# Optimization experiments

Measured on AMD Instinct MI355X. Metric: run time of the kernel, lower is better.

## Reference

```python
import jax, jax.numpy as jnp
import numpy as np

# ---- constants mirroring the torch module ----
OSAMP = 8            # temporal oversampling factor
MAX_ITER = 10        # forward solver iterations (LBFGS replaced by fixed GD)
NEG_SHIFT = 2 * OSAMP
OTP = 5              # baseline frames subtracted from ctc/aif
C_SHARP = 500.0      # sharpness constant C=500 in fermi_ir_func
LR = 0.1             # fixed step size for the deterministic forward solve


def interp_linear_1d(x, size):
    # interp_linear_1D: linear upsampling along last (time) axis
    return jax.image.resize(x, x.shape[:-1] + (size,), method='linear')


def fermi_ir(eta, t_os):
    # eta: [B,3,H,W] = (amplitude A, decay rate k, delay t0); t_os: [Tos]
    tsh = t_os - t_os[NEG_SHIFT]                    # negative time shift
    A = eta[:, 0][..., None]                        # [B,H,W,1]
    k = eta[:, 1][..., None]
    t0 = eta[:, 2][..., None]
    step = jax.nn.sigmoid(C_SHARP * tsh)            # sharp causal onset (C=500)
    return A * jax.nn.sigmoid(k * (t0 - tsh)) * step  # [B,H,W,Tos]


def convolve(aif, ir):
    # linear convolution along time via FFT; output aligned with neg_shift offset
    Tos = ir.shape[-1]
    n = 2 * Tos
    Fa = jnp.fft.rfft(aif, n=n, axis=-1)            # [B,1,1,n/2+1]
    Fi = jnp.fft.rfft(ir, n=n, axis=-1)             # [B,H,W,n/2+1]
    full = jnp.fft.irfft(Fa * Fi, n=n, axis=-1)
    return jax.lax.dynamic_slice_in_dim(full, NEG_SHIFT, Tos, axis=-1)


def make_objective(ctc, aif, time, eta_prior, lambda_reg):
    # preprocessing from FermiDataConsLBFGS.forward
    aif = aif - aif[..., :OTP].mean(-1, keepdims=True)
    ctc = ctc - ctc[..., :OTP].mean(-1, keepdims=True)
    Tos = OSAMP * ctc.shape[-1]
    aif_os = interp_linear_1d(aif, Tos)
    ctc_os = interp_linear_1d(ctc, Tos)
    t_os = interp_linear_1d(time, Tos)
    ctc_dc = ctc_os[..., ::OSAMP]                   # [B,H,W,T]
    C_nn = (eta_prior ** 2).sum(axis=(0, 2, 3), keepdims=True)  # [1,3,1,1]
    C_dc = (ctc_dc ** 2).sum()
    sp_lam = jax.nn.softplus(lambda_reg).squeeze()

    def F_obj(eta):  # FermiDConsObj.__call__ (OD disabled: indx_dc = all frames)
        ir = fermi_ir(eta, t_os)
        ctc_est = convolve(aif_os, ir)[..., ::OSAMP] / OSAMP
        dc = ((ctc_dc - ctc_est) ** 2 / C_dc).sum()
        reg = sp_lam * (((eta - eta_prior) ** 2) / C_nn).sum()
        pos = (jax.nn.relu(-eta) ** 2).sum()
        return dc + reg + pos
    return F_obj


def setup_inputs():
    key = jax.random.key(0)
    k1, k2, k3, k4 = jax.random.split(key, 4)
    B, H, W, T = 1, 128, 128, 64
    ctc = jax.random.normal(k1, (B, H, W, T), jnp.float32) * 0.1
    aif = jax.random.uniform(k2, (B, 1, 1, T), jnp.float32)
    time = jnp.arange(T, dtype=jnp.float32)
    seg = jnp.ones((B, H, W), jnp.int32)
    eta_nn = jax.random.uniform(k3, (B, 3, H, W), jnp.float32)
    lambda_reg = jax.random.normal(k4, (1,), jnp.float32)
    return {"ctc": ctc, "aif": aif, "time": time, "seg": seg,
            "eta_nn": eta_nn, "lambda_reg": lambda_reg}


def reference(ctc, aif, time, seg, eta_nn, lambda_reg):
    # seg only affects the (disabled) outlier-detection path
    F_obj = make_objective(ctc, aif, time, eta_nn, lambda_reg)
    gradF = jax.grad(F_obj)

    def step(eta, _):
        return eta - LR * gradF(eta), None

    eta_pi, _ = jax.lax.scan(step, eta_nn, None, length=MAX_ITER)
    return eta_pi
```

## Files before the change

### kernel.cpp

```cpp
#include <hip/hip_runtime.h>
#include <math.h>

#define T_IN 64
#define NPIX 16384
#define MAX_ITER 10
#define NSLOT 43

typedef _Float16 half8_t __attribute__((ext_vector_type(8)));
typedef __fp16   fp16x2  __attribute__((ext_vector_type(2)));
typedef float    f32x4   __attribute__((ext_vector_type(4)));
typedef int      i32x4   __attribute__((ext_vector_type(4)));

union H8 { half8_t v; fp16x2 h2[4]; i32x4 i4; };

__device__ __forceinline__ float rcp_fast(float x) { return __builtin_amdgcn_rcpf(x); }

__constant__ constexpr int NTMIN[16] = {0,0,0,0,0,1,1,1,1,2,2,2,2,3,3,3};
__constant__ constexpr int TOFS[16]  = {0,4,8,12,16,20,23,26,29,32,34,36,38,40,41,42};

template<int KT>
__device__ __forceinline__ void buildTile(float T0, float nK, float r, int q,
        const float (&d10b)[16], const float (&tse0)[8], const float (&tse15)[8],
        H8& F0h, H8& F1h, H8& F2h) {
    float  x[8];
    fp16x2 d1h[4];
    float  d10 = T0 - d10b[KT];
    const fp16x2 c1 = {(__fp16)0.25f, (__fp16)0.25f};
    const fp16x2 c2 = {(__fp16)0.50f, (__fp16)0.50f};
    const fp16x2 c3 = {(__fp16)0.75f, (__fp16)0.75f};
    bool arith = true;
    if constexpr (KT == 0 || KT == 15) {
        bool flat = (KT == 0) ? (q == 0) : (q == 3);
        if (flat) {
            arith = false;
            const float* te;
            if constexpr (KT == 0) te = tse0; else te = tse15;
            #pragma unroll
            for (int j = 0; j < 8; ++j) x[j] = __expf(nK * (T0 - te[j]));
            #pragma unroll
            for (int jj = 0; jj < 4; ++jj)
                d1h[jj] = __builtin_amdgcn_cvt_pkrtz(T0 - te[2*jj],
                                                     T0 - te[2*jj+1]);
        }
    }
    if (arith) {
        x[0] = __expf(nK * d10);
        x[4] = __expf(nK * (d10 - 0.5f));
        x[1] = x[0]*r; x[2] = x[1]*r; x[3] = x[2]*r;
        x[5] = x[4]*r; x[6] = x[5]*r; x[7] = x[6]*r;
        fp16x2 D0 = __builtin_amdgcn_cvt_pkrtz(d10, d10 - 0.125f);
        d1h[0] = D0;
        d1h[1] = D0 - c1;
        d1h[2] = D0 - c2;
        d1h[3] = D0 - c3;
    }
    #pragma unroll
    for (int jj = 0; jj < 4; ++jj) {
        float s1a = rcp_fast(1.0f + x[2*jj]);
        float s1b = rcp_fast(1.0f + x[2*jj+1]);
        fp16x2 sh = __builtin_amdgcn_cvt_pkrtz(s1a, s1b);
        fp16x2 eh = sh - sh*sh;
        F0h.h2[jj] = sh;
        F1h.h2[jj] = eh * d1h[jj];
        F2h.h2[jj] = eh;
    }
}

template<int KT>
struct Pipe2 {
    static __device__ __forceinline__ void run(float T0, float nK, float r, int q, int lane,
            const float (&d10b)[16], const float (&tse0)[8], const float (&tse15)[8],
            const i32x4* __restrict__ Bs,
            H8 (&F0p)[2], H8 (&F1p)[2], H8 (&F2p)[2],
            f32x4 (&acc)[3][4]) {
        constexpr int PB = (KT >> 1) & 1;
        if constexpr (KT + 2 < 16)
            buildTile<KT+2>(T0, nK, r, q, d10b, tse0, tse15,
                            F0p[PB^1], F1p[PB^1], F2p[PB^1]);
        const f32x4 Z = (f32x4){0.f, 0.f, 0.f, 0.f};
        #pragma unroll
        for (int nt = NTMIN[KT]; nt < 4; ++nt) {
            int slot = TOFS[KT] + nt - NTMIN[KT];
            H8 bh; bh.i4 = Bs[slot*64 + lane];
            if constexpr (KT < 2) {
                acc[0][nt] = __builtin_amdgcn_mfma_f32_16x16x32_f16(F0p[PB].v, bh.v, Z, 0, 0, 0);
                acc[1][nt] = __builtin_amdgcn_mfma_f32_16x16x32_f16(F1p[PB].v, bh.v, Z, 0, 0, 0);
                acc[2][nt] = __builtin_amdgcn_mfma_f32_16x16x32_f16(F2p[PB].v, bh.v, Z, 0, 0, 0);
            } else {
                acc[0][nt] = __builtin_amdgcn_mfma_f32_16x16x32_f16(F0p[PB].v, bh.v, acc[0][nt], 0, 0, 0);
                acc[1][nt] = __builtin_amdgcn_mfma_f32_16x16x32_f16(F1p[PB].v, bh.v, acc[1][nt], 0, 0, 0);
                acc[2][nt] = __builtin_amdgcn_mfma_f32_16x16x32_f16(F2p[PB].v, bh.v, acc[2][nt], 0, 0, 0);
            }
        }
        if constexpr (KT + 2 < 16)
            Pipe2<KT+2>::run(T0, nK, r, q, lane, d10b, tse0, tse15, Bs, F0p, F1p, F2p, acc);
    }
};

template<int H>
__device__ __forceinline__ void pipeAcc(float T0, float nK, float r, int q, int lane,
        const float (&d10b)[16], const float (&tse0)[8], const float (&tse15)[8],
        const i32x4* __restrict__ Bs, f32x4 (&acc)[3][4]) {
    H8 F0p[2], F1p[2], F2p[2];
    buildTile<H>(T0, nK, r, q, d10b, tse0, tse15, F0p[0], F1p[0], F2p[0]);
    Pipe2<H>::run(T0, nK, r, q, lane, d10b, tse0, tse15, Bs, F0p, F1p, F2p, acc);
}

template<int H>
__device__ __forceinline__ void sendHalf(const f32x4 (&acc)[3][4],
        float2* __restrict__ xch, int pair, int lane) {
    constexpr int SB = 2 - 2*H;
    float2* xw = xch + ((pair*2 + H)*12)*64 + lane;
    #pragma unroll
    for (int i = 0; i < 3; ++i)
        #pragma unroll
        for (int nt = 0; nt < 4; ++nt)
            xw[(i*4+nt)*64] = make_float2(acc[i][nt][SB], acc[i][nt][SB+1]);
}

template<int H>
__device__ __forceinline__ void finishDots(f32x4 (&acc)[3][4],
        const float2* __restrict__ xch, float (&Gtab)[4][16][4],
        int pair, int lane, int q, int n,
        const float (&dcreg)[4][4], float A) {
    constexpr int KB = 2*H;
    const float2* xr = xch + ((pair*2 + (1-H))*12)*64 + lane;
    #pragma unroll
    for (int i = 0; i < 3; ++i)
        #pragma unroll
        for (int nt = 0; nt < 4; ++nt) {
            float2 v = xr[(i*4+nt)*64];
            acc[i][nt][KB]   += v.x;
            acc[i][nt][KB+1] += v.y;
        }
    float Ap0 = __shfl(A, q*4 + KB);
    float Ap1 = __shfl(A, q*4 + KB + 1);
    float SA0=0.f,SK0=0.f,ST0=0.f, SA1=0.f,SK1=0.f,ST1=0.f;
    #pragma unroll
    for (int nt = 0; nt < 4; ++nt) {
        float Y0 = acc[0][nt][KB], Y1 = acc[1][nt][KB], Y2 = acc[2][nt][KB];
        float rr = fmaf(Ap0, Y0, -dcreg[nt][KB]);
        SA0 = fmaf(rr, Y0, SA0); SK0 = fmaf(rr, Y1, SK0); ST0 = fmaf(rr, Y2, ST0);
        float y0 = acc[0][nt][KB+1], y1 = acc[1][nt][KB+1], y2 = acc[2][nt][KB+1];
        float r2 = fmaf(Ap1, y0, -dcreg[nt][KB+1]);
        SA1 = fmaf(r2, y0, SA1); SK1 = fmaf(r2, y1, SK1); ST1 = fmaf(r2, y2, ST1);
    }
    #pragma unroll
    for (int m = 1; m < 16; m <<= 1) {
        SA0 += __shfl_xor(SA0, m); SK0 += __shfl_xor(SK0, m); ST0 += __shfl_xor(ST0, m);
        SA1 += __shfl_xor(SA1, m); SK1 += __shfl_xor(SK1, m); ST1 += __shfl_xor(ST1, m);
    }
    if (n == 0) {
        float* g = Gtab[pair][q*4 + KB];
        g[0] = SA0; g[1] = SK0; g[2] = ST0;
    }
    if (n == 1) {
        float* g = Gtab[pair][q*4 + KB + 1];
        g[0] = SA1; g[1] = SK1; g[2] = ST1;
    }
}

__global__ __launch_bounds__(256, 1) void k_prep(
        const float* __restrict__ ctc,  const float* __restrict__ aif,
        const float* __restrict__ timev,const float* __restrict__ eta,
        float* __restrict__ tshg, i32x4* __restrict__ Bg,
        f32x4* __restrict__ partials) {
    __shared__ float tshs[512];
    __shared__ float aifos[512];
    __shared__ float a_s[64], t_s[64];
    __shared__ f32x4 red[4];

    const int tid  = threadIdx.x;
    const int lane = tid & 63;
    const int wid  = tid >> 6;
    const int q = lane >> 4, n = lane & 15;
    const int pixbase = blockIdx.x * 64 + wid * 16;
    const int mypix   = pixbase + n;

    if (tid < 64) { a_s[tid] = aif[tid]; t_s[tid] = timev[tid]; }
    float A  = eta[mypix];
    float K  = eta[NPIX + mypix];
    float T0 = eta[2*NPIX + mypix];
    __syncthreads();
    {
        float m5a = 0.2f * (a_s[0]+a_s[1]+a_s[2]+a_s[3]+a_s[4]);
        float t16;
        {
            float xx = 1.5625f; int i0 = (int)xx; float f = xx - (float)i0;
            t16 = t_s[i0]*(1.0f-f) + t_s[i0+1]*f;
        }
        #pragma unroll
        for (int rep = 0; rep < 2; ++rep) {
            int i = tid + 256*rep;
            float x = ((float)i - 3.5f) * 0.125f;
            float ao, to;
            if (x <= 0.0f)       { ao = a_s[0]  - m5a; to = t_s[0];  }
            else if (x >= 63.0f) { ao = a_s[63] - m5a; to = t_s[63]; }
            else {
                int i0 = (int)x; float f = x - (float)i0;
                ao = (a_s[i0]-m5a)*(1.0f-f) + (a_s[i0+1]-m5a)*f;
                to = t_s[i0]*(1.0f-f) + t_s[i0+1]*f;
            }
            aifos[i] = ao;
            tshs[i]  = to - t16;
            if (blockIdx.x == 0) tshg[i] = to - t16;
        }
    }
    __syncthreads();

    if (blockIdx.x < NSLOT && tid < 64) {
        int slot = blockIdx.x, l = tid;
        int kt, nt;
        if (slot < 20)      { kt = slot >> 2; nt = slot & 3; }
        else if (slot < 32) { int s = slot - 20; int d3 = s / 3; kt = 5 + d3; nt = 1 + (s - 3*d3); }
        else if (slot < 40) { int s = slot - 32; kt = 9 + (s >> 1); nt = 2 + (s & 1); }
        else                { kt = 13 + (slot - 40); nt = 3; }
        int kbase = 32*kt + 8*(l >> 4);
        int m = 16 + 8 * (16*nt + (l & 15));
        H8 bh;
        #pragma unroll
        for (int jj = 0; jj < 4; ++jj) {
            float v[2];
            #pragma unroll
            for (int h = 0; h < 2; ++h) {
                int k  = kbase + 2*jj + h;
                int ai = m - k;
                float s2 = 1.0f / (1.0f + __expf(-500.0f * tshs[k]));
                v[h] = (ai >= 0 && ai < 512) ? s2 * aifos[ai] * 0.125f : 0.0f;
            }
            bh.h2[jj] = (fp16x2){(__fp16)v[0], (__fp16)v[1]};
        }
        Bg[slot*64 + l] = bh.i4;
    }

    float vs = 0.f;
    #pragma unroll
    for (int reg = 0; reg < 4; ++reg) {
        const float* cp = ctc + (pixbase + q*4 + reg) * T_IN;
        float m5 = 0.2f * (cp[0]+cp[1]+cp[2]+cp[3]+cp[4]);
        #pragma unroll
        for (int nt = 0; nt < 4; ++nt) {
            int d = nt*16 + n;
            float cc = cp[d] - m5;
            float cm = cp[(d > 0) ? d-1 : 0] - m5;
            float dc = (d == 0) ? cc : (0.4375f*cm + 0.5625f*cc);
            vs += dc * dc;
        }
    }
    {
        f32x4 pv = (f32x4){vs, 0.25f*A*A, 0.25f*K*K, 0.25f*T0*T0};
        #pragma unroll
        for (int m = 1; m < 64; m <<= 1) {
            pv.x += __shfl_xor(pv.x, m); pv.y += __shfl_xor(pv.y, m);
            pv.z += __shfl_xor(pv.z, m); pv.w += __shfl_xor(pv.w, m);
        }
        if (lane == 0) red[wid] = pv;
    }
    __syncthreads();
    if (tid == 0)
        partials[blockIdx.x] = red[0] + red[1] + red[2] + red[3];
}

__global__ __launch_bounds__(512, 2) void k_iter(
        const float* __restrict__ ctc,  const float* __restrict__ lam,
        const float* __restrict__ eta,  const float* __restrict__ tshg,
        const i32x4* __restrict__ Bg,   const f32x4* __restrict__ partials,
        float* __restrict__ out) {
    __shared__ i32x4 Bs[NSLOT * 64];
    __shared__ float tshs[512];
    __shared__ float2 xch[2*4*12*64];
    __shared__ float Gtab[4][16][4];

    const int tid  = threadIdx.x;
    const int lane = tid & 63;
    const int wid  = tid >> 6;
    const int hh   = wid & 1;
    const int pair = wid >> 1;
    const int q = lane >> 4, n = lane & 15;
    const int pixbase = blockIdx.x * 64 + pair * 16;
    const int mypix   = pixbase + n;

    for (int idx = tid; idx < NSLOT * 64; idx += 512) Bs[idx] = Bg[idx];
    tshs[tid] = tshg[tid];

    float A  = eta[mypix];
    float K  = eta[NPIX + mypix];
    float T0 = eta[2*NPIX + mypix];
    const float pA = A, pK = K, pT = T0;

    float dcreg[4][4];
    #pragma unroll
    for (int reg = 0; reg < 4; ++reg) {
        const float* cp = ctc + (pixbase + q*4 + reg) * T_IN;
        float m5 = 0.2f * (cp[0]+cp[1]+cp[2]+cp[3]+cp[4]);
        #pragma unroll
        for (int nt = 0; nt < 4; ++nt) {
            int d = nt*16 + n;
            float cc = cp[d] - m5;
            float cm = cp[(d > 0) ? d-1 : 0] - m5;
            dcreg[nt][reg] = (d == 0) ? cc : (0.4375f*cm + 0.5625f*cc);
        }
    }

    f32x4 tot = partials[lane] + partials[64+lane] + partials[128+lane]
              + partials[192+lane];
    #pragma unroll
    for (int m = 1; m < 64; m <<= 1) {
        tot.x += __shfl_xor(tot.x, m); tot.y += __shfl_xor(tot.y, m);
        tot.z += __shfl_xor(tot.z, m); tot.w += __shfl_xor(tot.w, m);
    }
    float spl;
    {
        float xl = lam[0];
        spl = (xl > 0.0f) ? (xl + log1pf(__expf(-xl))) : log1pf(__expf(xl));
    }
    const float cdc2 = 2.0f / tot.x;
    const float rgA  = 2.0f * spl / tot.y;
    const float rgK  = 2.0f * spl / tot.z;
    const float rgT  = 2.0f * spl / tot.w;

    __syncthreads();

    float  d10b[16];
    float  tse0[8], tse15[8];
    #pragma unroll
    for (int kt = 0; kt < 16; ++kt) d10b[kt] = tshs[32*kt + 8*q];
    #pragma unroll
    for (int j = 0; j < 8; ++j) { tse0[j] = tshs[8*q + j]; tse15[j] = tshs[480 + 8*q + j]; }

    #pragma unroll 1
    for (int it = 0; it < MAX_ITER; ++it) {
        float nK = -K;
        float r  = __expf(0.125f * K);

        f32x4 acc[3][4];
        if (hh == 0) {
            pipeAcc<0>(T0, nK, r, q, lane, d10b, tse0, tse15, Bs, acc);
            sendHalf<0>(acc, xch, pair, lane);
        } else {
            pipeAcc<1>(T0, nK, r, q, lane, d10b, tse0, tse15, Bs, acc);
            sendHalf<1>(acc, xch, pair, lane);
        }
        __syncthreads();
        if (hh == 0) finishDots<0>(acc, xch, Gtab, pair, lane, q, n, dcreg, A);
        else         finishDots<1>(acc, xch, Gtab, pair, lane, q, n, dcreg, A);
        __syncthreads();

        const float GA = Gtab[pair][n][0];
        const float GK = Gtab[pair][n][1];
        const float GT = Gtab[pair][n][2];
        float gA = fmaf(rgA, A  - pA, cdc2 * GA)         + 2.0f * fminf(A,  0.f);
        float gK = fmaf(rgK, K  - pK, cdc2 * A * GK)     + 2.0f * fminf(K,  0.f);
        float gT = fmaf(rgT, T0 - pT, cdc2 * A * K * GT) + 2.0f * fminf(T0, 0.f);
        A  -= 0.1f * gA;
        K  -= 0.1f * gK;
        T0 -= 0.1f * gT;
    }

    if (hh == 0 && lane < 16) {
        out[mypix]          = A;
        out[NPIX + mypix]   = K;
        out[2*NPIX + mypix] = T0;
    }
}

extern "C" void kernel_launch(void* const* d_in, const int* in_sizes, int n_in,
                              void* d_out, int out_size, void* d_ws, size_t ws_size,
                              hipStream_t stream) {
    const float* ctc   = (const float*)d_in[0];
    const float* aif   = (const float*)d_in[1];
    const float* timev = (const float*)d_in[2];
    const float* eta   = (const float*)d_in[4];
    const float* lam   = (const float*)d_in[5];
    float* out = (float*)d_out;
    f32x4* partials = (f32x4*)d_ws;
    float* tshg     = (float*)((char*)d_ws + 4096);
    i32x4* Bg       = (i32x4*)((char*)d_ws + 8192);

    k_prep<<<NPIX / 64, 256, 0, stream>>>(ctc, aif, timev, eta,
                                          tshg, Bg, partials);
    k_iter<<<NPIX / 64, 512, 0, stream>>>(ctc, lam, eta, tshg, Bg,
                                          partials, out);
}
```

Baseline: 106.5 us.

## Split MFMA work by output columns and drop accumulator exchange barrier

```diff
diff --git a/kernel.cpp b/kernel.cpp
--- a/kernel.cpp
+++ b/kernel.cpp
@@ -15,8 +15,9 @@
 
 __device__ __forceinline__ float rcp_fast(float x) { return __builtin_amdgcn_rcpf(x); }
 
-__constant__ constexpr int NTMIN[16] = {0,0,0,0,0,1,1,1,1,2,2,2,2,3,3,3};
-__constant__ constexpr int TOFS[16]  = {0,4,8,12,16,20,23,26,29,32,34,36,38,40,41,42};
+__constant__ constexpr int NTMIN[16]  = {0,0,0,0,0,1,1,1,1,2,2,2,2,3,3,3};
+__constant__ constexpr int TOFS[16]   = {0,4,8,12,16,20,23,26,29,32,34,36,38,40,41,42};
+__constant__ constexpr int LASTKT[4]  = {4,8,12,15};
 
 template<int KT>
 __device__ __forceinline__ void buildTile(float T0, float nK, float r, int q,
@@ -66,98 +67,59 @@
     }
 }
 
-template<int KT>
-struct Pipe2 {
+template<int H, int KT>
+struct PipeN {
+    static constexpr int NA   = (H == 0) ? 0 : 1;
+    static constexpr int NB   = (H == 0) ? 3 : 2;
+    static constexpr int LAST = (H == 0) ? 15 : 12;
     static __device__ __forceinline__ void run(float T0, float nK, float r, int q, int lane,
             const float (&d10b)[16], const float (&tse0)[8], const float (&tse15)[8],
             const i32x4* __restrict__ Bs,
             H8 (&F0p)[2], H8 (&F1p)[2], H8 (&F2p)[2],
-            f32x4 (&acc)[3][4]) {
-        constexpr int PB = (KT >> 1) & 1;
-        if constexpr (KT + 2 < 16)
-            buildTile<KT+2>(T0, nK, r, q, d10b, tse0, tse15,
+            f32x4 (&acc)[3][2]) {
+        constexpr int PB = KT & 1;
+        if constexpr (KT + 1 <= LAST)
+            buildTile<KT+1>(T0, nK, r, q, d10b, tse0, tse15,
                             F0p[PB^1], F1p[PB^1], F2p[PB^1]);
         const f32x4 Z = (f32x4){0.f, 0.f, 0.f, 0.f};
-        #pragma unroll
-        for (int nt = NTMIN[KT]; nt < 4; ++nt) {
-            int slot = TOFS[KT] + nt - NTMIN[KT];
+        if constexpr (KT <= LASTKT[NA]) {
+            constexpr int slot = TOFS[KT] + NA - NTMIN[KT];
             H8 bh; bh.i4 = Bs[slot*64 + lane];
-            if constexpr (KT < 2) {
-                acc[0][nt] = __builtin_amdgcn_mfma_f32_16x16x32_f16(F0p[PB].v, bh.v, Z, 0, 0, 0);
-                acc[1][nt] = __builtin_amdgcn_mfma_f32_16x16x32_f16(F1p[PB].v, bh.v, Z, 0, 0, 0);
-                acc[2][nt] = __builtin_amdgcn_mfma_f32_16x16x32_f16(F2p[PB].v, bh.v, Z, 0, 0, 0);
+            if constexpr (KT == 0) {
+                acc[0][0] = __builtin_amdgcn_mfma_f32_16x16x32_f16(F0p[PB].v, bh.v, Z, 0, 0, 0);
+                acc[1][0] = __builtin_amdgcn_mfma_f32_16x16x32_f16(F1p[PB].v, bh.v, Z, 0, 0, 0);
+                acc[2][0] = __builtin_amdgcn_mfma_f32_16x16x32_f16(F2p[PB].v, bh.v, Z, 0, 0, 0);
             } else {
-                acc[0][nt] = __builtin_amdgcn_mfma_f32_16x16x32_f16(F0p[PB].v, bh.v, acc[0][nt], 0, 0, 0);
-                acc[1][nt] = __builtin_amdgcn_mfma_f32_16x16x32_f16(F1p[PB].v, bh.v, acc[1][nt], 0, 0, 0);
-                acc[2][nt] = __builtin_amdgcn_mfma_f32_16x16x32_f16(F2p[PB].v, bh.v, acc[2][nt], 0, 0, 0);
-            }
-        }
-        if constexpr (KT + 2 < 16)
-            Pipe2<KT+2>::run(T0, nK, r, q, lane, d10b, tse0, tse15, Bs, F0p, F1p, F2p, acc);
+                acc[0][0] = __builtin_amdgcn_mfma_f32_16x16x32_f16(F0p[PB].v, bh.v, acc[0][0], 0, 0, 0);
+                acc[1][0] = __builtin_amdgcn_mfma_f32_16x16x32_f16(F1p[PB].v, bh.v, acc[1][0], 0, 0, 0);
+                acc[2][0] = __builtin_amdgcn_mfma_f32_16x16x32_f16(F2p[PB].v, bh.v, acc[2][0], 0, 0, 0);
+            }
+        }
+        if constexpr (KT <= LASTKT[NB]) {
+            constexpr int slot = TOFS[KT] + NB - NTMIN[KT];
+            H8 bh; bh.i4 = Bs[slot*64 + lane];
+            if constexpr (KT == 0) {
+                acc[0][1] = __builtin_amdgcn_mfma_f32_16x16x32_f16(F0p[PB].v, bh.v, Z, 0, 0, 0);
+                acc[1][1] = __builtin_amdgcn_mfma_f32_16x16x32_f16(F1p[PB].v, bh.v, Z, 0, 0, 0);
+                acc[2][1] = __builtin_amdgcn_mfma_f32_16x16x32_f16(F2p[PB].v, bh.v, Z, 0, 0, 0);
+            } else {
+                acc[0][1] = __builtin_amdgcn_mfma_f32_16x16x32_f16(F0p[PB].v, bh.v, acc[0][1], 0, 0, 0);
+                acc[1][1] = __builtin_amdgcn_mfma_f32_16x16x32_f16(F1p[PB].v, bh.v, acc[1][1], 0, 0, 0);
+                acc[2][1] = __builtin_amdgcn_mfma_f32_16x16x32_f16(F2p[PB].v, bh.v, acc[2][1], 0, 0, 0);
+            }
+        }
+        if constexpr (KT + 1 <= LAST)
+            PipeN<H, KT+1>::run(T0, nK, r, q, lane, d10b, tse0, tse15, Bs, F0p, F1p, F2p, acc);
     }
 };
 
 template<int H>
 __device__ __forceinline__ void pipeAcc(float T0, float nK, float r, int q, int lane,
         const float (&d10b)[16], const float (&tse0)[8], const float (&tse15)[8],
-        const i32x4* __restrict__ Bs, f32x4 (&acc)[3][4]) {
+        const i32x4* __restrict__ Bs, f32x4 (&acc)[3][2]) {
     H8 F0p[2], F1p[2], F2p[2];
-    buildTile<H>(T0, nK, r, q, d10b, tse0, tse15, F0p[0], F1p[0], F2p[0]);
-    Pipe2<H>::run(T0, nK, r, q, lane, d10b, tse0, tse15, Bs, F0p, F1p, F2p, acc);
-}
-
-template<int H>
-__device__ __forceinline__ void sendHalf(const f32x4 (&acc)[3][4],
-        float2* __restrict__ xch, int pair, int lane) {
-    constexpr int SB = 2 - 2*H;
-    float2* xw = xch + ((pair*2 + H)*12)*64 + lane;
-    #pragma unroll
-    for (int i = 0; i < 3; ++i)
-        #pragma unroll
-        for (int nt = 0; nt < 4; ++nt)
-            xw[(i*4+nt)*64] = make_float2(acc[i][nt][SB], acc[i][nt][SB+1]);
-}
-
-template<int H>
-__device__ __forceinline__ void finishDots(f32x4 (&acc)[3][4],
-        const float2* __restrict__ xch, float (&Gtab)[4][16][4],
-        int pair, int lane, int q, int n,
-        const float (&dcreg)[4][4], float A) {
-    constexpr int KB = 2*H;
-    const float2* xr = xch + ((pair*2 + (1-H))*12)*64 + lane;
-    #pragma unroll
-    for (int i = 0; i < 3; ++i)
-        #pragma unroll
-        for (int nt = 0; nt < 4; ++nt) {
-            float2 v = xr[(i*4+nt)*64];
-            acc[i][nt][KB]   += v.x;
-            acc[i][nt][KB+1] += v.y;
-        }
-    float Ap0 = __shfl(A, q*4 + KB);
-    float Ap1 = __shfl(A, q*4 + KB + 1);
-    float SA0=0.f,SK0=0.f,ST0=0.f, SA1=0.f,SK1=0.f,ST1=0.f;
-    #pragma unroll
-    for (int nt = 0; nt < 4; ++nt) {
-        float Y0 = acc[0][nt][KB], Y1 = acc[1][nt][KB], Y2 = acc[2][nt][KB];
-        float rr = fmaf(Ap0, Y0, -dcreg[nt][KB]);
-        SA0 = fmaf(rr, Y0, SA0); SK0 = fmaf(rr, Y1, SK0); ST0 = fmaf(rr, Y2, ST0);
-        float y0 = acc[0][nt][KB+1], y1 = acc[1][nt][KB+1], y2 = acc[2][nt][KB+1];
-        float r2 = fmaf(Ap1, y0, -dcreg[nt][KB+1]);
-        SA1 = fmaf(r2, y0, SA1); SK1 = fmaf(r2, y1, SK1); ST1 = fmaf(r2, y2, ST1);
-    }
-    #pragma unroll
-    for (int m = 1; m < 16; m <<= 1) {
-        SA0 += __shfl_xor(SA0, m); SK0 += __shfl_xor(SK0, m); ST0 += __shfl_xor(ST0, m);
-        SA1 += __shfl_xor(SA1, m); SK1 += __shfl_xor(SK1, m); ST1 += __shfl_xor(ST1, m);
-    }
-    if (n == 0) {
-        float* g = Gtab[pair][q*4 + KB];
-        g[0] = SA0; g[1] = SK0; g[2] = ST0;
-    }
-    if (n == 1) {
-        float* g = Gtab[pair][q*4 + KB + 1];
-        g[0] = SA1; g[1] = SK1; g[2] = ST1;
-    }
+    buildTile<0>(T0, nK, r, q, d10b, tse0, tse15, F0p[0], F1p[0], F2p[0]);
+    PipeN<H, 0>::run(T0, nK, r, q, lane, d10b, tse0, tse15, Bs, F0p, F1p, F2p, acc);
 }
 
 __global__ __launch_bounds__(256, 1) void k_prep(
@@ -261,44 +223,48 @@
         partials[blockIdx.x] = red[0] + red[1] + red[2] + red[3];
 }
 
-__global__ __launch_bounds__(512, 2) void k_iter(
+__global__ __launch_bounds__(256, 2) void k_iter(
         const float* __restrict__ ctc,  const float* __restrict__ lam,
         const float* __restrict__ eta,  const float* __restrict__ tshg,
         const i32x4* __restrict__ Bg,   const f32x4* __restrict__ partials,
         float* __restrict__ out) {
     __shared__ i32x4 Bs[NSLOT * 64];
     __shared__ float tshs[512];
-    __shared__ float2 xch[2*4*12*64];
-    __shared__ float Gtab[4][16][4];
+    __shared__ float xs[2][2][2][4][12];
 
     const int tid  = threadIdx.x;
     const int lane = tid & 63;
     const int wid  = tid >> 6;
     const int hh   = wid & 1;
-    const int pair = wid >> 1;
+    const int pairid = wid >> 1;
     const int q = lane >> 4, n = lane & 15;
-    const int pixbase = blockIdx.x * 64 + pair * 16;
+    const int pixbase = blockIdx.x * 32 + pairid * 16;
     const int mypix   = pixbase + n;
 
-    for (int idx = tid; idx < NSLOT * 64; idx += 512) Bs[idx] = Bg[idx];
+    for (int idx = tid; idx < NSLOT * 64; idx += 256) Bs[idx] = Bg[idx];
     tshs[tid] = tshg[tid];
+    if (tid < 256) tshs[tid + 256] = tshg[tid + 256];
 
     float A  = eta[mypix];
     float K  = eta[NPIX + mypix];
     float T0 = eta[2*NPIX + mypix];
     const float pA = A, pK = K, pT = T0;
 
-    float dcreg[4][4];
+    const int ntA = hh ? 1 : 0;
+    const int ntB = hh ? 2 : 3;
+
+    float dcreg[2][4];
     #pragma unroll
     for (int reg = 0; reg < 4; ++reg) {
         const float* cp = ctc + (pixbase + q*4 + reg) * T_IN;
         float m5 = 0.2f * (cp[0]+cp[1]+cp[2]+cp[3]+cp[4]);
         #pragma unroll
-        for (int nt = 0; nt < 4; ++nt) {
+        for (int L = 0; L < 2; ++L) {
+            int nt = L ? ntB : ntA;
             int d = nt*16 + n;
             float cc = cp[d] - m5;
             float cm = cp[(d > 0) ? d-1 : 0] - m5;
-            dcreg[nt][reg] = (d == 0) ? cc : (0.4375f*cm + 0.5625f*cc);
+            dcreg[L][reg] = (d == 0) ? cc : (0.4375f*cm + 0.5625f*cc);
         }
     }
 
@@ -333,22 +299,65 @@
         float nK = -K;
         float r  = __expf(0.125f * K);
 
-        f32x4 acc[3][4];
-        if (hh == 0) {
-            pipeAcc<0>(T0, nK, r, q, lane, d10b, tse0, tse15, Bs, acc);
-            sendHalf<0>(acc, xch, pair, lane);
-        } else {
-            pipeAcc<1>(T0, nK, r, q, lane, d10b, tse0, tse15, Bs, acc);
-            sendHalf<1>(acc, xch, pair, lane);
+        f32x4 acc[3][2];
+        if (hh == 0) pipeAcc<0>(T0, nK, r, q, lane, d10b, tse0, tse15, Bs, acc);
+        else         pipeAcc<1>(T0, nK, r, q, lane, d10b, tse0, tse15, Bs, acc);
+
+        float Ap[4];
+        #pragma unroll
+        for (int r2 = 0; r2 < 4; ++r2) Ap[r2] = __shfl(A, q*4 + r2);
+        float SA[4], SK[4], ST[4];
+        #pragma unroll
+        for (int r2 = 0; r2 < 4; ++r2) { SA[r2]=0.f; SK[r2]=0.f; ST[r2]=0.f; }
+        #pragma unroll
+        for (int L = 0; L < 2; ++L)
+            #pragma unroll
+            for (int r2 = 0; r2 < 4; ++r2) {
+                float Y0 = acc[0][L][r2], Y1 = acc[1][L][r2], Y2 = acc[2][L][r2];
+                float rr = fmaf(Ap[r2], Y0, -dcreg[L][r2]);
+                SA[r2] = fmaf(rr, Y0, SA[r2]);
+                SK[r2] = fmaf(rr, Y1, SK[r2]);
+                ST[r2] = fmaf(rr, Y2, ST[r2]);
+            }
+        #pragma unroll
+        for (int r2 = 0; r2 < 4; ++r2)
+            #pragma unroll
+            for (int m = 1; m < 16; m <<= 1) {
+                SA[r2] += __shfl_xor(SA[r2], m);
+                SK[r2] += __shfl_xor(SK[r2], m);
+                ST[r2] += __shfl_xor(ST[r2], m);
+            }
+
+        if (n == 0) {
+            float* xp = &xs[it & 1][pairid][hh][q][0];
+            #pragma unroll
+            for (int r2 = 0; r2 < 4; ++r2) {
+                xp[r2]   = SA[r2];
+                xp[4+r2] = SK[r2];
+                xp[8+r2] = ST[r2];
+            }
         }
         __syncthreads();
-        if (hh == 0) finishDots<0>(acc, xch, Gtab, pair, lane, q, n, dcreg, A);
-        else         finishDots<1>(acc, xch, Gtab, pair, lane, q, n, dcreg, A);
-        __syncthreads();
-
-        const float GA = Gtab[pair][n][0];
-        const float GK = Gtab[pair][n][1];
-        const float GT = Gtab[pair][n][2];
+        {
+            const float* xo = &xs[it & 1][pairid][1 - hh][q][0];
+            #pragma unroll
+            for (int r2 = 0; r2 < 4; ++r2) {
+                SA[r2] += xo[r2];
+                SK[r2] += xo[4+r2];
+                ST[r2] += xo[8+r2];
+            }
+        }
+
+        int src = (n >> 2) * 16;
+        float GA = 0.f, GK = 0.f, GT = 0.f;
+        #pragma unroll
+        for (int r2 = 0; r2 < 4; ++r2) {
+            float tA = __shfl(SA[r2], src);
+            float tK = __shfl(SK[r2], src);
+            float tT = __shfl(ST[r2], src);
+            if ((n & 3) == r2) { GA = tA; GK = tK; GT = tT; }
+        }
+
         float gA = fmaf(rgA, A  - pA, cdc2 * GA)         + 2.0f * fminf(A,  0.f);
         float gK = fmaf(rgK, K  - pK, cdc2 * A * GK)     + 2.0f * fminf(K,  0.f);
         float gT = fmaf(rgT, T0 - pT, cdc2 * A * K * GT) + 2.0f * fminf(T0, 0.f);
@@ -379,6 +388,6 @@
 
     k_prep<<<NPIX / 64, 256, 0, stream>>>(ctc, aif, timev, eta,
                                           tshg, Bg, partials);
-    k_iter<<<NPIX / 64, 512, 0, stream>>>(ctc, lam, eta, tshg, Bg,
+    k_iter<<<NPIX / 32, 256, 0, stream>>>(ctc, lam, eta, tshg, Bg,
                                           partials, out);
 }
```

Result: slower. 119.3 us (+12.1%).

## Split K-dimension across four waves per pixel group, read B from global

Applied to the files above, without the earlier changes.

```diff
diff --git a/kernel.cpp b/kernel.cpp
--- a/kernel.cpp
+++ b/kernel.cpp
@@ -20,7 +20,7 @@
 
 template<int KT>
 __device__ __forceinline__ void buildTile(float T0, float nK, float r, int q,
-        const float (&d10b)[16], const float (&tse0)[8], const float (&tse15)[8],
+        const float (&d10b)[16], const float (&tse)[8],
         H8& F0h, H8& F1h, H8& F2h) {
     float  x[8];
     fp16x2 d1h[4];
@@ -33,14 +33,12 @@
         bool flat = (KT == 0) ? (q == 0) : (q == 3);
         if (flat) {
             arith = false;
-            const float* te;
-            if constexpr (KT == 0) te = tse0; else te = tse15;
             #pragma unroll
-            for (int j = 0; j < 8; ++j) x[j] = __expf(nK * (T0 - te[j]));
+            for (int j = 0; j < 8; ++j) x[j] = __expf(nK * (T0 - tse[j]));
             #pragma unroll
             for (int jj = 0; jj < 4; ++jj)
-                d1h[jj] = __builtin_amdgcn_cvt_pkrtz(T0 - te[2*jj],
-                                                     T0 - te[2*jj+1]);
+                d1h[jj] = __builtin_amdgcn_cvt_pkrtz(T0 - tse[2*jj],
+                                                     T0 - tse[2*jj+1]);
         }
     }
     if (arith) {
@@ -67,96 +65,74 @@
 }
 
 template<int KT>
-struct Pipe2 {
-    static __device__ __forceinline__ void run(float T0, float nK, float r, int q, int lane,
-            const float (&d10b)[16], const float (&tse0)[8], const float (&tse15)[8],
-            const i32x4* __restrict__ Bs,
+struct Pipe4 {
+    static __device__ __forceinline__ void run(float T0, float nK, float r, int q,
+            const float (&d10b)[16], const float (&tse)[8],
+            const i32x4* __restrict__ Bgl,
             H8 (&F0p)[2], H8 (&F1p)[2], H8 (&F2p)[2],
             f32x4 (&acc)[3][4]) {
-        constexpr int PB = (KT >> 1) & 1;
-        if constexpr (KT + 2 < 16)
-            buildTile<KT+2>(T0, nK, r, q, d10b, tse0, tse15,
+        constexpr int PB = (KT >> 2) & 1;
+        H8 bh[4];
+        #pragma unroll
+        for (int nt = NTMIN[KT]; nt < 4; ++nt)
+            bh[nt].i4 = Bgl[(TOFS[KT] + nt - NTMIN[KT]) * 64];
+        if constexpr (KT + 4 < 16)
+            buildTile<KT+4>(T0, nK, r, q, d10b, tse,
                             F0p[PB^1], F1p[PB^1], F2p[PB^1]);
         const f32x4 Z = (f32x4){0.f, 0.f, 0.f, 0.f};
         #pragma unroll
         for (int nt = NTMIN[KT]; nt < 4; ++nt) {
-            int slot = TOFS[KT] + nt - NTMIN[KT];
-            H8 bh; bh.i4 = Bs[slot*64 + lane];
-            if constexpr (KT < 2) {
-                acc[0][nt] = __builtin_amdgcn_mfma_f32_16x16x32_f16(F0p[PB].v, bh.v, Z, 0, 0, 0);
-                acc[1][nt] = __builtin_amdgcn_mfma_f32_16x16x32_f16(F1p[PB].v, bh.v, Z, 0, 0, 0);
-                acc[2][nt] = __builtin_amdgcn_mfma_f32_16x16x32_f16(F2p[PB].v, bh.v, Z, 0, 0, 0);
+            if constexpr (KT < 4) {
+                acc[0][nt] = __builtin_amdgcn_mfma_f32_16x16x32_f16(F0p[PB].v, bh[nt].v, Z, 0, 0, 0);
+                acc[1][nt] = __builtin_amdgcn_mfma_f32_16x16x32_f16(F1p[PB].v, bh[nt].v, Z, 0, 0, 0);
+                acc[2][nt] = __builtin_amdgcn_mfma_f32_16x16x32_f16(F2p[PB].v, bh[nt].v, Z, 0, 0, 0);
             } else {
-                acc[0][nt] = __builtin_amdgcn_mfma_f32_16x16x32_f16(F0p[PB].v, bh.v, acc[0][nt], 0, 0, 0);
-                acc[1][nt] = __builtin_amdgcn_mfma_f32_16x16x32_f16(F1p[PB].v, bh.v, acc[1][nt], 0, 0, 0);
-                acc[2][nt] = __builtin_amdgcn_mfma_f32_16x16x32_f16(F2p[PB].v, bh.v, acc[2][nt], 0, 0, 0);
+                acc[0][nt] = __builtin_amdgcn_mfma_f32_16x16x32_f16(F0p[PB].v, bh[nt].v, acc[0][nt], 0, 0, 0);
+                acc[1][nt] = __builtin_amdgcn_mfma_f32_16x16x32_f16(F1p[PB].v, bh[nt].v, acc[1][nt], 0, 0, 0);
+                acc[2][nt] = __builtin_amdgcn_mfma_f32_16x16x32_f16(F2p[PB].v, bh[nt].v, acc[2][nt], 0, 0, 0);
             }
         }
-        if constexpr (KT + 2 < 16)
-            Pipe2<KT+2>::run(T0, nK, r, q, lane, d10b, tse0, tse15, Bs, F0p, F1p, F2p, acc);
+        if constexpr (KT + 4 < 16)
+            Pipe4<KT+4>::run(T0, nK, r, q, d10b, tse, Bgl, F0p, F1p, F2p, acc);
     }
 };
 
 template<int H>
-__device__ __forceinline__ void pipeAcc(float T0, float nK, float r, int q, int lane,
-        const float (&d10b)[16], const float (&tse0)[8], const float (&tse15)[8],
-        const i32x4* __restrict__ Bs, f32x4 (&acc)[3][4]) {
+__device__ __forceinline__ void pipeAcc(float T0, float nK, float r, int q,
+        const float (&d10b)[16], const float (&tse)[8],
+        const i32x4* __restrict__ Bgl, f32x4 (&acc)[3][4]) {
     H8 F0p[2], F1p[2], F2p[2];
-    buildTile<H>(T0, nK, r, q, d10b, tse0, tse15, F0p[0], F1p[0], F2p[0]);
-    Pipe2<H>::run(T0, nK, r, q, lane, d10b, tse0, tse15, Bs, F0p, F1p, F2p, acc);
-}
-
-template<int H>
-__device__ __forceinline__ void sendHalf(const f32x4 (&acc)[3][4],
-        float2* __restrict__ xch, int pair, int lane) {
-    constexpr int SB = 2 - 2*H;
-    float2* xw = xch + ((pair*2 + H)*12)*64 + lane;
-    #pragma unroll
-    for (int i = 0; i < 3; ++i)
-        #pragma unroll
-        for (int nt = 0; nt < 4; ++nt)
-            xw[(i*4+nt)*64] = make_float2(acc[i][nt][SB], acc[i][nt][SB+1]);
-}
-
-template<int H>
-__device__ __forceinline__ void finishDots(f32x4 (&acc)[3][4],
-        const float2* __restrict__ xch, float (&Gtab)[4][16][4],
-        int pair, int lane, int q, int n,
-        const float (&dcreg)[4][4], float A) {
-    constexpr int KB = 2*H;
-    const float2* xr = xch + ((pair*2 + (1-H))*12)*64 + lane;
-    #pragma unroll
-    for (int i = 0; i < 3; ++i)
-        #pragma unroll
-        for (int nt = 0; nt < 4; ++nt) {
-            float2 v = xr[(i*4+nt)*64];
-            acc[i][nt][KB]   += v.x;
-            acc[i][nt][KB+1] += v.y;
-        }
-    float Ap0 = __shfl(A, q*4 + KB);
-    float Ap1 = __shfl(A, q*4 + KB + 1);
-    float SA0=0.f,SK0=0.f,ST0=0.f, SA1=0.f,SK1=0.f,ST1=0.f;
-    #pragma unroll
-    for (int nt = 0; nt < 4; ++nt) {
-        float Y0 = acc[0][nt][KB], Y1 = acc[1][nt][KB], Y2 = acc[2][nt][KB];
-        float rr = fmaf(Ap0, Y0, -dcreg[nt][KB]);
-        SA0 = fmaf(rr, Y0, SA0); SK0 = fmaf(rr, Y1, SK0); ST0 = fmaf(rr, Y2, ST0);
-        float y0 = acc[0][nt][KB+1], y1 = acc[1][nt][KB+1], y2 = acc[2][nt][KB+1];
-        float r2 = fmaf(Ap1, y0, -dcreg[nt][KB+1]);
-        SA1 = fmaf(r2, y0, SA1); SK1 = fmaf(r2, y1, SK1); ST1 = fmaf(r2, y2, ST1);
-    }
-    #pragma unroll
-    for (int m = 1; m < 16; m <<= 1) {
-        SA0 += __shfl_xor(SA0, m); SK0 += __shfl_xor(SK0, m); ST0 += __shfl_xor(ST0, m);
-        SA1 += __shfl_xor(SA1, m); SK1 += __shfl_xor(SK1, m); ST1 += __shfl_xor(ST1, m);
-    }
-    if (n == 0) {
-        float* g = Gtab[pair][q*4 + KB];
-        g[0] = SA0; g[1] = SK0; g[2] = ST0;
-    }
-    if (n == 1) {
-        float* g = Gtab[pair][q*4 + KB + 1];
-        g[0] = SA1; g[1] = SK1; g[2] = ST1;
+    buildTile<H>(T0, nK, r, q, d10b, tse, F0p[0], F1p[0], F2p[0]);
+    Pipe4<H>::run(T0, nK, r, q, d10b, tse, Bgl, F0p, F1p, F2p, acc);
+}
+
+template<int C>
+__device__ __forceinline__ void xsWrite(const f32x4 (&acc)[3][4],
+        float2 (&xs)[4][6][64], int lane) {
+    #pragma unroll
+    for (int j = 0; j < 6; ++j)
+        xs[C][j][lane] = make_float2(acc[j>>1][(j&1)*2][C],
+                                     acc[j>>1][(j&1)*2+1][C]);
+}
+template<int C>
+__device__ __forceinline__ void xsAccum(const f32x4 (&acc)[3][4],
+        float2 (&xs)[4][6][64], int lane) {
+    #pragma unroll
+    for (int j = 0; j < 6; ++j) {
+        float2 v = xs[C][j][lane];
+        v.x += acc[j>>1][(j&1)*2][C];
+        v.y += acc[j>>1][(j&1)*2+1][C];
+        xs[C][j][lane] = v;
+    }
+}
+template<int C>
+__device__ __forceinline__ void xsFinal(const f32x4 (&acc)[3][4],
+        const float2 (&xs)[4][6][64], int lane, float (&Yv)[3][4]) {
+    #pragma unroll
+    for (int j = 0; j < 6; ++j) {
+        float2 v = xs[C][j][lane];
+        Yv[j>>1][(j&1)*2]   = v.x + acc[j>>1][(j&1)*2][C];
+        Yv[j>>1][(j&1)*2+1] = v.y + acc[j>>1][(j&1)*2+1][C];
     }
 }
 
@@ -261,44 +237,38 @@
         partials[blockIdx.x] = red[0] + red[1] + red[2] + red[3];
 }
 
-__global__ __launch_bounds__(512, 2) void k_iter(
+__global__ __launch_bounds__(256, 4) void k_iter(
         const float* __restrict__ ctc,  const float* __restrict__ lam,
         const float* __restrict__ eta,  const float* __restrict__ tshg,
         const i32x4* __restrict__ Bg,   const f32x4* __restrict__ partials,
         float* __restrict__ out) {
-    __shared__ i32x4 Bs[NSLOT * 64];
-    __shared__ float tshs[512];
-    __shared__ float2 xch[2*4*12*64];
-    __shared__ float Gtab[4][16][4];
+    __shared__ float2 xs[4][6][64];
+    __shared__ float  Gtab[16][4];
 
     const int tid  = threadIdx.x;
     const int lane = tid & 63;
-    const int wid  = tid >> 6;
-    const int hh   = wid & 1;
-    const int pair = wid >> 1;
+    const int hh   = tid >> 6;
     const int q = lane >> 4, n = lane & 15;
-    const int pixbase = blockIdx.x * 64 + pair * 16;
+    const int pixbase = blockIdx.x * 16;
     const int mypix   = pixbase + n;
 
-    for (int idx = tid; idx < NSLOT * 64; idx += 512) Bs[idx] = Bg[idx];
-    tshs[tid] = tshg[tid];
+    const i32x4* Bgl = Bg + lane;
 
     float A  = eta[mypix];
     float K  = eta[NPIX + mypix];
     float T0 = eta[2*NPIX + mypix];
     const float pA = A, pK = K, pT = T0;
 
-    float dcreg[4][4];
-    #pragma unroll
-    for (int reg = 0; reg < 4; ++reg) {
-        const float* cp = ctc + (pixbase + q*4 + reg) * T_IN;
+    float dch[4];
+    {
+        const float* cp = ctc + (pixbase + q*4 + hh) * T_IN;
         float m5 = 0.2f * (cp[0]+cp[1]+cp[2]+cp[3]+cp[4]);
         #pragma unroll
         for (int nt = 0; nt < 4; ++nt) {
             int d = nt*16 + n;
             float cc = cp[d] - m5;
             float cm = cp[(d > 0) ? d-1 : 0] - m5;
-            dcreg[nt][reg] = (d == 0) ? cc : (0.4375f*cm + 0.5625f*cc);
+            dch[nt] = (d == 0) ? cc : (0.4375f*cm + 0.5625f*cc);
         }
     }
 
@@ -319,14 +289,15 @@
     const float rgK  = 2.0f * spl / tot.z;
     const float rgT  = 2.0f * spl / tot.w;
 
-    __syncthreads();
-
-    float  d10b[16];
-    float  tse0[8], tse15[8];
-    #pragma unroll
-    for (int kt = 0; kt < 16; ++kt) d10b[kt] = tshs[32*kt + 8*q];
-    #pragma unroll
-    for (int j = 0; j < 8; ++j) { tse0[j] = tshs[8*q + j]; tse15[j] = tshs[480 + 8*q + j]; }
+    float d10b[16];
+    #pragma unroll
+    for (int kt = 0; kt < 16; ++kt) d10b[kt] = tshg[32*kt + 8*q];
+    float tse[8];
+    {
+        const float* tb = (hh == 3) ? (tshg + 480) : tshg;
+        #pragma unroll
+        for (int j = 0; j < 8; ++j) tse[j] = tb[8*q + j];
+    }
 
     #pragma unroll 1
     for (int it = 0; it < MAX_ITER; ++it) {
@@ -334,21 +305,64 @@
         float r  = __expf(0.125f * K);
 
         f32x4 acc[3][4];
-        if (hh == 0) {
-            pipeAcc<0>(T0, nK, r, q, lane, d10b, tse0, tse15, Bs, acc);
-            sendHalf<0>(acc, xch, pair, lane);
-        } else {
-            pipeAcc<1>(T0, nK, r, q, lane, d10b, tse0, tse15, Bs, acc);
-            sendHalf<1>(acc, xch, pair, lane);
+        if      (hh == 0) pipeAcc<0>(T0, nK, r, q, d10b, tse, Bgl, acc);
+        else if (hh == 1) pipeAcc<1>(T0, nK, r, q, d10b, tse, Bgl, acc);
+        else if (hh == 2) pipeAcc<2>(T0, nK, r, q, d10b, tse, Bgl, acc);
+        else              pipeAcc<3>(T0, nK, r, q, d10b, tse, Bgl, acc);
+
+        switch (hh) {
+            case 0: xsWrite<1>(acc, xs, lane); break;
+            case 1: xsWrite<2>(acc, xs, lane); break;
+            case 2: xsWrite<3>(acc, xs, lane); break;
+            default: xsWrite<0>(acc, xs, lane); break;
         }
         __syncthreads();
-        if (hh == 0) finishDots<0>(acc, xch, Gtab, pair, lane, q, n, dcreg, A);
-        else         finishDots<1>(acc, xch, Gtab, pair, lane, q, n, dcreg, A);
+        switch (hh) {
+            case 0: xsAccum<2>(acc, xs, lane); break;
+            case 1: xsAccum<3>(acc, xs, lane); break;
+            case 2: xsAccum<0>(acc, xs, lane); break;
+            default: xsAccum<1>(acc, xs, lane); break;
+        }
         __syncthreads();
-
-        const float GA = Gtab[pair][n][0];
-        const float GK = Gtab[pair][n][1];
-        const float GT = Gtab[pair][n][2];
+        switch (hh) {
+            case 0: xsAccum<3>(acc, xs, lane); break;
+            case 1: xsAccum<0>(acc, xs, lane); break;
+            case 2: xsAccum<1>(acc, xs, lane); break;
+            default: xsAccum<2>(acc, xs, lane); break;
+        }
+        __syncthreads();
+        float Yv[3][4];
+        switch (hh) {
+            case 0: xsFinal<0>(acc, xs, lane, Yv); break;
+            case 1: xsFinal<1>(acc, xs, lane, Yv); break;
+            case 2: xsFinal<2>(acc, xs, lane, Yv); break;
+            default: xsFinal<3>(acc, xs, lane, Yv); break;
+        }
+
+        float Ap = __shfl(A, q*4 + hh);
+        float SA = 0.f, SK = 0.f, ST = 0.f;
+        #pragma unroll
+        for (int nt = 0; nt < 4; ++nt) {
+            float Y0 = Yv[0][nt], Y1 = Yv[1][nt], Y2 = Yv[2][nt];
+            float rr = fmaf(Ap, Y0, -dch[nt]);
+            SA = fmaf(rr, Y0, SA);
+            SK = fmaf(rr, Y1, SK);
+            ST = fmaf(rr, Y2, ST);
+        }
+        #pragma unroll
+        for (int m = 1; m < 16; m <<= 1) {
+            SA += __shfl_xor(SA, m); SK += __shfl_xor(SK, m); ST += __shfl_xor(ST, m);
+        }
+        if (n == 0) {
+            Gtab[q*4 + hh][0] = SA;
+            Gtab[q*4 + hh][1] = SK;
+            Gtab[q*4 + hh][2] = ST;
+        }
+        __syncthreads();
+
+        const float GA = Gtab[n][0];
+        const float GK = Gtab[n][1];
+        const float GT = Gtab[n][2];
         float gA = fmaf(rgA, A  - pA, cdc2 * GA)         + 2.0f * fminf(A,  0.f);
         float gK = fmaf(rgK, K  - pK, cdc2 * A * GK)     + 2.0f * fminf(K,  0.f);
         float gT = fmaf(rgT, T0 - pT, cdc2 * A * K * GT) + 2.0f * fminf(T0, 0.f);
@@ -379,6 +393,6 @@
 
     k_prep<<<NPIX / 64, 256, 0, stream>>>(ctc, aif, timev, eta,
                                           tshg, Bg, partials);
-    k_iter<<<NPIX / 64, 512, 0, stream>>>(ctc, lam, eta, tshg, Bg,
+    k_iter<<<NPIX / 16, 256, 0, stream>>>(ctc, lam, eta, tshg, Bg,
                                           partials, out);
 }
```

Measured after the change: 153.1 us. 43.7% more time.
